# Optimization experiments

Hardware: AMD Instinct MI355X
Metric: run time of the kernel (lower is better)

The kernel has to match this reference:

```python
import jax, jax.numpy as jnp
import numpy as np

K = 11        # filter_size
HALF = K // 2 # 5
N_ITER = 5
EPS = 1e-8


def setup_inputs() -> dict:
    key = jax.random.key(0)
    k1, k2 = jax.random.split(key)
    logits = jax.random.normal(k1, (16, 100000), dtype=jnp.float32)
    p = jax.random.normal(k2, (16, 100000, 3), dtype=jnp.float32)
    return {"logits": logits, "p": p}


def _shift_stack(x, offsets, n):
    # x: [B, C, N+2*HALF] padded; returns [B, len(offsets), C, N]
    return jnp.stack([x[:, :, d:d + n] for d in offsets], axis=1)


def reference(logits, p):
    B, N = logits.shape
    feat = jnp.transpose(p, (0, 2, 1))      # [B,3,N]  (p.permute(0,2,1))
    unary = logits[:, None, :]              # [B,1,N]  (logits.unsqueeze(1))

    offsets = [d for d in range(K) if d != HALF]  # exclude self-connection

    fpad = jnp.pad(feat, ((0, 0), (0, 0), (HALF, HALF)))
    mpad = jnp.pad(jnp.ones((B, 1, N), logits.dtype), ((0, 0), (0, 0), (HALF, HALF)))
    f_sh = _shift_stack(fpad, offsets, N)   # [B,10,3,N]
    m_sh = _shift_stack(mpad, offsets, N)   # [B,10,1,N] valid mask (zero outside seq)

    # Gaussian pairwise kernel on point features, fixed across iterations
    w = jnp.exp(-0.5 * jnp.sum((feat[:, None] - f_sh) ** 2, axis=2, keepdims=True)) * m_sh  # [B,10,1,N]
    wsum = jnp.sum(w, axis=1) + EPS         # [B,1,N]

    def body(q, _):
        qpad = jnp.pad(q, ((0, 0), (0, 0), (HALF, HALF)))
        q_sh = _shift_stack(qpad, offsets, N)          # [B,10,1,N]
        msg = jnp.sum(w * q_sh, axis=1) / wsum          # normalized message
        q_new = jax.nn.sigmoid(unary + msg)             # mean-field update
        return q_new, None

    q0 = jax.nn.sigmoid(unary)
    q, _ = jax.lax.scan(body, q0, None, length=N_ITER)
    return q[:, 0, :]  # .squeeze() -> [B,N] marginal probabilities
```

## Files before the change

### kernel.cpp

```cpp
#include <hip/hip_runtime.h>


constexpr int BLK   = 256;
constexpr int WPB   = 4;
constexpr int G     = 4;
constexpr int E     = 64 * G;
constexpr int HL    = 28;
constexpr int C     = E - 2 * HL;
constexpr int NITER = 5;
constexpr int N_    = 100000;
constexpr int CPB   = (N_ + C - 1) / C;
constexpr float EPS = 1e-8f;

__device__ __forceinline__ float frcp(float x) { return __builtin_amdgcn_rcpf(x); }
__device__ __forceinline__ float sigm(float x) { return frcp(1.0f + __expf(-x)); }

__global__ __launch_bounds__(BLK, 8) void crf_kernel(
    const float* __restrict__ logits, const float* __restrict__ p,
    float* __restrict__ out)
{
  const int lane  = threadIdx.x & 63;
  const int wid   = threadIdx.x >> 6;
  const int tile  = blockIdx.x * WPB + wid;
  const int b     = tile / CPB;
  const int chunk = tile - b * CPB;
  const int s0    = chunk * C - HL;
  const int gb    = s0 + G * lane;
  const float* lg = logits + (size_t)b * N_;
  const float* pp = p + (size_t)b * N_ * 3;

  const bool interior = (s0 >= 5) && (s0 + E + 5 < N_);

  float own[12], un[G];
  if (interior) {
    const float4* vp = (const float4*)(pp + 3 * gb);
    float4 v0 = vp[0], v1 = vp[1], v2 = vp[2];
    own[0] = v0.x; own[1]  = v0.y; own[2]  = v0.z; own[3]  = v0.w;
    own[4] = v1.x; own[5]  = v1.y; own[6]  = v1.z; own[7]  = v1.w;
    own[8] = v2.x; own[9]  = v2.y; own[10] = v2.z; own[11] = v2.w;
    float4 u = *(const float4*)(lg + gb);
    un[0] = u.x; un[1] = u.y; un[2] = u.z; un[3] = u.w;
  } else {
    #pragma unroll
    for (int k = 0; k < G; ++k) {
      int gc = min(max(gb + k, 0), N_ - 1);
      own[3 * k + 0] = pp[3 * (size_t)gc + 0];
      own[3 * k + 1] = pp[3 * (size_t)gc + 1];
      own[3 * k + 2] = pp[3 * (size_t)gc + 2];
      un[k] = lg[gc];
    }
  }

  float fh[5][3];
  #pragma unroll
  for (int j = 0; j < 4; ++j)
    #pragma unroll
    for (int c = 0; c < 3; ++c)
      fh[j][c] = __shfl_down(own[3 * j + c], 1);
  #pragma unroll
  for (int c = 0; c < 3; ++c)
    fh[4][c] = __shfl_down(own[c], 2);

  float ww[G][5];
  #pragma unroll
  for (int k = 0; k < G; ++k) {
    #pragma unroll
    for (int d = 0; d < 5; ++d) {
      const int j = k + d + 1;
      float p0 = (j < 4) ? own[3 * j + 0] : fh[j - 4][0];
      float p1 = (j < 4) ? own[3 * j + 1] : fh[j - 4][1];
      float p2 = (j < 4) ? own[3 * j + 2] : fh[j - 4][2];
      float d0 = own[3 * k + 0] - p0;
      float d1 = own[3 * k + 1] - p1;
      float d2 = own[3 * k + 2] - p2;
      float ex = __expf(-0.5f * (d0 * d0 + d1 * d1 + d2 * d2));
      if (!interior)
        ex = (gb + k >= 0 && gb + k + d + 1 < N_) ? ex : 0.0f;
      ww[k][d] = ex;
    }
  }

  float wl[G][5];
  #pragma unroll
  for (int k = 0; k < G; ++k) {
    #pragma unroll
    for (int d = 0; d < 5; ++d) {
      const int s = k - d - 1;
      float v;
      if (s >= 0)       v = ww[s][d];
      else if (s >= -4) v = __shfl_up(ww[s + 4][d], 1);
      else              v = __shfl_up(ww[3][d], 2);
      wl[k][d] = v;
    }
  }

  float q[G];
  #pragma unroll
  for (int k = 0; k < G; ++k) {
    float ws = EPS;
    #pragma unroll
    for (int d = 0; d < 5; ++d) ws += ww[k][d] + wl[k][d];
    float inv = frcp(ws);
    #pragma unroll
    for (int d = 0; d < 5; ++d) { ww[k][d] *= inv; wl[k][d] *= inv; }
    q[k] = sigm(un[k]);
  }

  #pragma unroll
  for (int it = 0; it < NITER; ++it) {
    float qx[14];
    qx[0] = __shfl_up(q[3], 2);
    #pragma unroll
    for (int j = 0; j < 4; ++j) qx[1 + j] = __shfl_up(q[j], 1);
    #pragma unroll
    for (int k = 0; k < G; ++k) qx[5 + k] = q[k];
    #pragma unroll
    for (int j = 0; j < 4; ++j) qx[9 + j] = __shfl_down(q[j], 1);
    qx[13] = __shfl_down(q[0], 2);

    #pragma unroll
    for (int k = 0; k < G; ++k) {
      float acc = un[k];
      #pragma unroll
      for (int d = 0; d < 5; ++d) {
        acc += wl[k][d] * qx[5 + k - d - 1];
        acc += ww[k][d] * qx[5 + k + d + 1];
      }
      q[k] = sigm(acc);
    }
  }

  const int e0 = G * lane;
  if (e0 >= HL && e0 + G <= E - HL) {
    const int gx = chunk * C + (e0 - HL);
    float* ob = out + (size_t)b * N_ + gx;
    float4 v = make_float4(q[0], q[1], q[2], q[3]);
    if (gx + 3 < N_) {
      *(float4*)ob = v;
    } else {
      #pragma unroll
      for (int j = 0; j < 4; ++j)
        if (gx + j < N_) ob[j] = (&v.x)[j];
    }
  }
}

extern "C" void kernel_launch(void* const* d_in, const int* in_sizes, int n_in,
                              void* d_out, int out_size, void* d_ws, size_t ws_size,
                              hipStream_t stream) {
  const float* logits = (const float*)d_in[0];
  const float* p      = (const float*)d_in[1];
  float* out          = (float*)d_out;
  const int B = in_sizes[0] / N_;
  const int total_tiles = B * CPB;
  dim3 grid(total_tiles / WPB), block(BLK);
  crf_kernel<<<grid, block, 0, stream>>>(logits, p, out);
}
```

Baseline: 18.40 us.

## Process two tiles per single-wave workgroup with both loads issued up front

Each workgroup is now one 64-lane wave that handles two tiles, issuing the global loads for both before computing either, so memory latency for the second tile overlaps compute on the first. Batch size is hardcoded to 16 and the grid halved, with launch bounds changed to 256-thread-equivalent occupancy hint 4. This raises register pressure and relies on TILES being even and B fixed at 16.

```diff
diff --git a/kernel.cpp b/kernel.cpp
--- a/kernel.cpp
+++ b/kernel.cpp
@@ -1,8 +1,7 @@
 #include <hip/hip_runtime.h>
 
 
-constexpr int BLK   = 256;
-constexpr int WPB   = 4;
+constexpr int BLK   = 64;
 constexpr int G     = 4;
 constexpr int E     = 64 * G;
 constexpr int HL    = 28;
@@ -10,28 +9,25 @@
 constexpr int NITER = 5;
 constexpr int N_    = 100000;
 constexpr int CPB   = (N_ + C - 1) / C;
+constexpr int TILES = 16 * CPB;
+constexpr int NWG   = TILES / 2;
 constexpr float EPS = 1e-8f;
 
 __device__ __forceinline__ float frcp(float x) { return __builtin_amdgcn_rcpf(x); }
 __device__ __forceinline__ float sigm(float x) { return frcp(1.0f + __expf(-x)); }
 
-__global__ __launch_bounds__(BLK, 8) void crf_kernel(
+__device__ __forceinline__ void load_tile(
+    int tile, int lane,
     const float* __restrict__ logits, const float* __restrict__ p,
-    float* __restrict__ out)
+    float own[12], float un[4], int& gb, int& bb, int& chunk, bool& interior)
 {
-  const int lane  = threadIdx.x & 63;
-  const int wid   = threadIdx.x >> 6;
-  const int tile  = blockIdx.x * WPB + wid;
-  const int b     = tile / CPB;
-  const int chunk = tile - b * CPB;
-  const int s0    = chunk * C - HL;
-  const int gb    = s0 + G * lane;
-  const float* lg = logits + (size_t)b * N_;
-  const float* pp = p + (size_t)b * N_ * 3;
-
-  const bool interior = (s0 >= 5) && (s0 + E + 5 < N_);
-
-  float own[12], un[G];
+  bb    = tile / CPB;
+  chunk = tile - bb * CPB;
+  const int s0 = chunk * C - HL;
+  gb = s0 + G * lane;
+  const float* lg = logits + (size_t)bb * N_;
+  const float* pp = p + (size_t)bb * N_ * 3;
+  interior = (s0 >= 5) && (s0 + E + 5 < N_);
   if (interior) {
     const float4* vp = (const float4*)(pp + 3 * gb);
     float4 v0 = vp[0], v1 = vp[1], v2 = vp[2];
@@ -50,7 +46,13 @@
       un[k] = lg[gc];
     }
   }
+}
 
+__device__ __forceinline__ void process_tile(
+    const float own[12], const float un[4],
+    int gb, int bb, int chunk, bool interior, int lane,
+    float* __restrict__ out)
+{
   float fh[5][3];
   #pragma unroll
   for (int j = 0; j < 4; ++j)
@@ -133,7 +135,7 @@
   const int e0 = G * lane;
   if (e0 >= HL && e0 + G <= E - HL) {
     const int gx = chunk * C + (e0 - HL);
-    float* ob = out + (size_t)b * N_ + gx;
+    float* ob = out + (size_t)bb * N_ + gx;
     float4 v = make_float4(q[0], q[1], q[2], q[3]);
     if (gx + 3 < N_) {
       *(float4*)ob = v;
@@ -145,14 +147,31 @@
   }
 }
 
+__global__ __launch_bounds__(BLK, 4) void crf_kernel(
+    const float* __restrict__ logits, const float* __restrict__ p,
+    float* __restrict__ out)
+{
+  const int lane = threadIdx.x;
+  const int tA   = blockIdx.x;
+  const int tB   = blockIdx.x + NWG;
+
+  float ownA[12], unA[4], ownB[12], unB[4];
+  int gbA, bA, chA, gbB, bB, chB;
+  bool intA, intB;
+
+  load_tile(tA, lane, logits, p, ownA, unA, gbA, bA, chA, intA);
+  load_tile(tB, lane, logits, p, ownB, unB, gbB, bB, chB, intB);
+
+  process_tile(ownA, unA, gbA, bA, chA, intA, lane, out);
+  process_tile(ownB, unB, gbB, bB, chB, intB, lane, out);
+}
+
 extern "C" void kernel_launch(void* const* d_in, const int* in_sizes, int n_in,
                               void* d_out, int out_size, void* d_ws, size_t ws_size,
                               hipStream_t stream) {
   const float* logits = (const float*)d_in[0];
   const float* p      = (const float*)d_in[1];
   float* out          = (float*)d_out;
-  const int B = in_sizes[0] / N_;
-  const int total_tiles = B * CPB;
-  dim3 grid(total_tiles / WPB), block(BLK);
+  dim3 grid(NWG), block(BLK);
   crf_kernel<<<grid, block, 0, stream>>>(logits, p, out);
 }
```

Measured after the change: 17.98 us. 2.3% less time.
